# Kernel optimization log

Hardware: AMD Instinct MI355X
Metric: run time of the kernel (lower is better)

Reference implementation:

```python
import jax, jax.numpy as jnp
import numpy as np

N = 50000   # nodes
E = 800000  # edges (before self loops)
NEG_SLOPE = 0.2
EPS_BN = 1e-5
EPS_SM = 1e-16  # PyG softmax denominator epsilon


def gat_conv(x, src, dst, W, att_src, att_dst, bias, heads, ch):
    n = x.shape[0]
    xh = (x @ W).reshape(n, heads, ch)                       # [N,H,C]
    a_src = jnp.sum(xh * att_src, axis=-1)                   # [N,H]
    a_dst = jnp.sum(xh * att_dst, axis=-1)                   # [N,H]
    e = a_src[src] + a_dst[dst]                              # [E,H]
    e = jax.nn.leaky_relu(e, NEG_SLOPE)
    m = jax.ops.segment_max(e, dst, num_segments=n)          # segment softmax
    ex = jnp.exp(e - m[dst])
    denom = jax.ops.segment_sum(ex, dst, num_segments=n)
    alpha = ex / (denom[dst] + EPS_SM)                       # [E,H]
    msg = alpha[:, :, None] * xh[src]                        # [E,H,C]
    out = jax.ops.segment_sum(msg, dst, num_segments=n)      # [N,H,C]
    return out.reshape(n, heads * ch) + bias


def batch_norm(x, gamma, beta):
    mu = jnp.mean(x, axis=0)
    var = jnp.mean((x - mu) ** 2, axis=0)
    return (x - mu) * jax.lax.rsqrt(var + EPS_BN) * gamma + beta


def setup_inputs() -> dict:
    key = jax.random.key(0)
    ks = jax.random.split(key, 16)
    d = {}
    d['x'] = jax.random.normal(ks[0], (N, 128), jnp.float32)
    d['edge_index'] = jax.random.randint(ks[1], (2, E), 0, N, dtype=jnp.int64)
    d['W1'] = jax.random.normal(ks[2], (128, 256), jnp.float32) * 0.1
    d['as1'] = jax.random.normal(ks[3], (2, 128), jnp.float32) * 0.1
    d['ad1'] = jax.random.normal(ks[4], (2, 128), jnp.float32) * 0.1
    d['b1'] = jax.random.normal(ks[5], (256,), jnp.float32) * 0.1
    d['g1'] = jnp.ones((256,), jnp.float32)
    d['be1'] = jnp.zeros((256,), jnp.float32)
    d['W2'] = jax.random.normal(ks[6], (256, 128), jnp.float32) * 0.1
    d['as2'] = jax.random.normal(ks[7], (2, 64), jnp.float32) * 0.1
    d['ad2'] = jax.random.normal(ks[8], (2, 64), jnp.float32) * 0.1
    d['b2'] = jax.random.normal(ks[9], (128,), jnp.float32) * 0.1
    d['g2'] = jnp.ones((128,), jnp.float32)
    d['be2'] = jnp.zeros((128,), jnp.float32)
    d['W3'] = jax.random.normal(ks[10], (128, 128), jnp.float32) * 0.1
    d['as3'] = jax.random.normal(ks[11], (2, 64), jnp.float32) * 0.1
    d['ad3'] = jax.random.normal(ks[12], (2, 64), jnp.float32) * 0.1
    d['b3'] = jax.random.normal(ks[13], (128,), jnp.float32) * 0.1
    d['lw'] = jax.random.normal(ks[14], (128, 64), jnp.float32) * 0.1
    d['lb'] = jnp.zeros((64,), jnp.float32)
    return d


def reference(x, edge_index, W1, as1, ad1, b1, g1, be1,
              W2, as2, ad2, b2, g2, be2,
              W3, as3, ad3, b3, lw, lb):
    # add self loops (PyG GATConv default add_self_loops=True)
    loops = jnp.arange(N, dtype=edge_index.dtype)
    src = jnp.concatenate([edge_index[0], loops])
    dst = jnp.concatenate([edge_index[1], loops])

    h = jax.nn.relu(gat_conv(x, src, dst, W1, as1, ad1, b1, 2, 128))   # [N,256]
    h = batch_norm(h, g1, be1)
    h = jax.nn.relu(gat_conv(h, src, dst, W2, as2, ad2, b2, 2, 64))    # [N,128]
    h = batch_norm(h, g2, be2)
    h = jax.nn.relu(gat_conv(h, src, dst, W3, as3, ad3, b3, 2, 64))    # [N,128]
    return h @ lw + lb                                                 # [N,64]
```

## Files before the change

kernel.cpp:

```cpp
#include <hip/hip_runtime.h>
#include <hip/hip_bf16.h>

#define NEG_SLOPE 0.2f
#define EPS_BN 1e-5f
#define EPS_SM 1e-16f
#define CAP 128

typedef __bf16 bf16x8 __attribute__((ext_vector_type(8)));
typedef __bf16 bf16x4 __attribute__((ext_vector_type(4)));
typedef float floatx4 __attribute__((ext_vector_type(4)));

__device__ __forceinline__ float leaky(float x) { return x > 0.f ? x : NEG_SLOPE * x; }

__global__ void k_init(const int* __restrict__ ei, int* __restrict__ flag,
                       int* __restrict__ zbase, int zwords, int e) {
    if (blockIdx.x == 0) {
        __shared__ int cnt_s[256];
        int i = threadIdx.x;
        int nz = (2 * i + 1 < 2 * e && ei[2 * i + 1] != 0) ? 1 : 0;
        cnt_s[i] = nz;
        __syncthreads();
        for (int off = 128; off > 0; off >>= 1) {
            if (i < off) cnt_s[i] += cnt_s[i + off];
            __syncthreads();
        }
        if (i == 0) *flag = (cnt_s[0] < 128) ? 1 : 0;
        return;
    }
    int g = (blockIdx.x - 1) * 256 + threadIdx.x;
    int stride = (gridDim.x - 1) * 256;
    for (int k = g; k < zwords; k += stride) zbase[k] = 0;
}

__global__ void k_hist_wconv(const int* __restrict__ ei, const int* __restrict__ flag,
                             int* __restrict__ deg, int* __restrict__ col, int e, int ebase,
                             const float* __restrict__ W1, __bf16* __restrict__ Wb1,
                             const float* __restrict__ W2, __bf16* __restrict__ Wb2,
                             const float* __restrict__ W3, __bf16* __restrict__ Wb3) {
    int g = threadIdx.x + blockIdx.x * blockDim.x;
    if (g < e) {
        bool is64 = (*flag) != 0;
        int s = is64 ? ei[2 * g] : ei[g];
        int d = is64 ? ei[2 * (e + g)] : ei[e + g];
        int r = atomicAdd(&deg[d], 1);
        if (r < CAP) col[((size_t)d << 7) + r] = s;
    } else {
        int idx = g - ebase;
        if (idx >= 0 && idx < 32768) {
            int mm = idx >> 7, kk = idx & 127;
            Wb1[idx] = (__bf16)W1[(size_t)kk * 256 + mm];
        } else if (idx < 65536) {
            int i2 = idx - 32768;
            int mm = i2 >> 8, kk = i2 & 255;
            Wb2[i2] = (__bf16)W2[(size_t)kk * 128 + mm];
        } else if (idx < 81920) {
            int i3 = idx - 65536;
            int mm = i3 >> 7, kk = i3 & 127;
            Wb3[i3] = (__bf16)W3[(size_t)kk * 128 + mm];
        }
    }
}

template <int K, int LC, bool BF16IN, int NT>
__global__ __launch_bounds__(256) void k_gemm(const void* __restrict__ Ain,
                                              const __bf16* __restrict__ Bt,
                                              __bf16* __restrict__ Cb, int n, int M,
                                              const float* __restrict__ bnsums,
                                              const float* __restrict__ gam,
                                              const float* __restrict__ bet,
                                              const float* __restrict__ att_s,
                                              const float* __restrict__ att_d,
                                              float* __restrict__ asrc,
                                              float* __restrict__ adst) {
    __shared__ __align__(16) __bf16 As[128][72];
    __shared__ __align__(16) __bf16 Bs[NT * 16][72];
    __shared__ float sc_lds[K], sh_lds[K];
    const int row0 = blockIdx.y * 128, col0 = blockIdx.x * (NT * 16);
    const int lane = threadIdx.x & 63, w = threadIdx.x >> 6;
    const int m = lane & 15, quad = lane >> 4;

    if (bnsums) {
        for (int c = threadIdx.x; c < K; c += 256) {
            float mean = bnsums[c] / n;
            float var = bnsums[256 + c] / n - mean * mean;
            float sc = gam[c] * rsqrtf(var + EPS_BN);
            sc_lds[c] = sc;
            sh_lds[c] = bet[c] - mean * sc;
        }
        __syncthreads();
    }

    floatx4 acc[2][NT];
#pragma unroll
    for (int i = 0; i < 2; ++i)
#pragma unroll
        for (int j = 0; j < NT; ++j) acc[i][j] = (floatx4)0.f;

    const int sr = threadIdx.x >> 1;
    const int sk = (threadIdx.x & 1) * 32;

    for (int kc = 0; kc < K; kc += 64) {
        {
            int grow = row0 + sr;
            if (grow < n) {
                if (BF16IN) {
                    const __bf16* p = (const __bf16*)Ain + (size_t)grow * K + kc + sk;
#pragma unroll
                    for (int q = 0; q < 4; ++q) {
                        bf16x8 vv = *reinterpret_cast<const bf16x8*>(p + q * 8);
                        if (bnsums) {
                            int c = kc + sk + q * 8;
                            bf16x8 r;
#pragma unroll
                            for (int e2 = 0; e2 < 8; ++e2)
                                r[e2] = (__bf16)((float)vv[e2] * sc_lds[c + e2] + sh_lds[c + e2]);
                            vv = r;
                        }
                        *reinterpret_cast<bf16x8*>(&As[sr][sk + q * 8]) = vv;
                    }
                } else {
                    const float* p = (const float*)Ain + (size_t)grow * K + kc + sk;
#pragma unroll
                    for (int q = 0; q < 8; ++q) {
                        float4 v = *reinterpret_cast<const float4*>(p + q * 4);
                        bf16x4 cv = {(__bf16)v.x, (__bf16)v.y, (__bf16)v.z, (__bf16)v.w};
                        *reinterpret_cast<bf16x4*>(&As[sr][sk + q * 4]) = cv;
                    }
                }
            } else {
#pragma unroll
                for (int q = 0; q < 4; ++q)
                    *reinterpret_cast<bf16x8*>(&As[sr][sk + q * 8]) = (bf16x8)(__bf16)0.f;
            }
        }
        if (NT == 8) {
            const __bf16* p = Bt + (size_t)(col0 + sr) * K + kc + sk;
#pragma unroll
            for (int q = 0; q < 4; ++q)
                *reinterpret_cast<bf16x8*>(&Bs[sr][sk + q * 8]) =
                    *reinterpret_cast<const bf16x8*>(p + q * 8);
        } else {
            int sr4 = threadIdx.x >> 2, sk4 = (threadIdx.x & 3) * 16;
            const __bf16* p = Bt + (size_t)(col0 + sr4) * K + kc + sk4;
            *reinterpret_cast<bf16x8*>(&Bs[sr4][sk4]) = *reinterpret_cast<const bf16x8*>(p);
            *reinterpret_cast<bf16x8*>(&Bs[sr4][sk4 + 8]) = *reinterpret_cast<const bf16x8*>(p + 8);
        }
        __syncthreads();
#pragma unroll
        for (int ks = 0; ks < 64; ks += 32) {
            bf16x8 a0 = *reinterpret_cast<const bf16x8*>(&As[w * 32 + m][ks + quad * 8]);
            bf16x8 a1 = *reinterpret_cast<const bf16x8*>(&As[w * 32 + 16 + m][ks + quad * 8]);
#pragma unroll
            for (int nt = 0; nt < NT; ++nt) {
                bf16x8 b = *reinterpret_cast<const bf16x8*>(&Bs[nt * 16 + m][ks + quad * 8]);
                acc[0][nt] = __builtin_amdgcn_mfma_f32_16x16x32_bf16(a0, b, acc[0][nt], 0, 0, 0);
                acc[1][nt] = __builtin_amdgcn_mfma_f32_16x16x32_bf16(a1, b, acc[1][nt], 0, 0, 0);
            }
        }
        __syncthreads();
    }
#pragma unroll
    for (int mt = 0; mt < 2; ++mt)
#pragma unroll
        for (int nt = 0; nt < NT; ++nt)
#pragma unroll
            for (int r = 0; r < 4; ++r) {
                int row = row0 + w * 32 + mt * 16 + quad * 4 + r;
                if (row < n) Cb[(size_t)row * M + col0 + nt * 16 + m] = (__bf16)acc[mt][nt][r];
            }
    {
        float asv[NT], adv[NT];
#pragma unroll
        for (int nt = 0; nt < NT; ++nt) {
            int c = col0 + nt * 16 + m;
            asv[nt] = att_s[c];
            adv[nt] = att_d[c];
        }
        const int h = (col0 >> LC) & 1;
#pragma unroll
        for (int mt = 0; mt < 2; ++mt)
#pragma unroll
            for (int r = 0; r < 4; ++r) {
                int row = row0 + w * 32 + mt * 16 + quad * 4 + r;
                float pa = 0.f, pb = 0.f;
#pragma unroll
                for (int nt = 0; nt < NT; ++nt) {
                    float v = acc[mt][nt][r];
                    pa += v * asv[nt];
                    pb += v * adv[nt];
                }
#pragma unroll
                for (int off = 1; off <= 8; off <<= 1) {
                    pa += __shfl_xor(pa, off);
                    pb += __shfl_xor(pb, off);
                }
                if (m == 0 && row < n) {
                    asrc[2 * row + h] = pa;
                    adst[2 * row + h] = pb;
                }
            }
    }
}

__global__ __launch_bounds__(256) void k_lin(const float* __restrict__ A,
                                             const float* __restrict__ lw,
                                             const float* __restrict__ lb,
                                             float* __restrict__ out, int n) {
    __shared__ __align__(16) __bf16 Ahi[64][136];
    __shared__ __align__(16) __bf16 Alo[64][136];
    __shared__ __align__(16) __bf16 Bhi[64][136];
    const int row0 = blockIdx.x * 64;
    const int lane = threadIdx.x & 63, w = threadIdx.x >> 6;
    const int m = lane & 15, quad = lane >> 4;
    floatx4 acc[4];
#pragma unroll
    for (int i = 0; i < 4; ++i) acc[i] = (floatx4)0.f;
    {
        int sr = threadIdx.x >> 2, sk0 = (threadIdx.x & 3) * 32;
        int grow = row0 + sr;
#pragma unroll
        for (int q = 0; q < 8; ++q) {
            float4 v = make_float4(0.f, 0.f, 0.f, 0.f);
            if (grow < n) v = *reinterpret_cast<const float4*>(A + (size_t)grow * 128 + sk0 + q * 4);
            float vv[4] = {v.x, v.y, v.z, v.w};
#pragma unroll
            for (int i = 0; i < 4; ++i) {
                __bf16 h = (__bf16)vv[i];
                Ahi[sr][sk0 + q * 4 + i] = h;
                Alo[sr][sk0 + q * 4 + i] = (__bf16)(vv[i] - (float)h);
            }
        }
    }
    {
        int k0 = threadIdx.x >> 1, m0 = (threadIdx.x & 1) * 32;
#pragma unroll
        for (int q = 0; q < 8; ++q) {
            float4 v = *reinterpret_cast<const float4*>(lw + (size_t)k0 * 64 + m0 + q * 4);
            float vv[4] = {v.x, v.y, v.z, v.w};
#pragma unroll
            for (int i = 0; i < 4; ++i) Bhi[m0 + q * 4 + i][k0] = (__bf16)vv[i];
        }
    }
    __syncthreads();
#pragma unroll
    for (int ks = 0; ks < 128; ks += 32) {
        bf16x8 ah = *reinterpret_cast<const bf16x8*>(&Ahi[w * 16 + m][ks + quad * 8]);
        bf16x8 al = *reinterpret_cast<const bf16x8*>(&Alo[w * 16 + m][ks + quad * 8]);
#pragma unroll
        for (int nt = 0; nt < 4; ++nt) {
            bf16x8 bh = *reinterpret_cast<const bf16x8*>(&Bhi[nt * 16 + m][ks + quad * 8]);
            acc[nt] = __builtin_amdgcn_mfma_f32_16x16x32_bf16(ah, bh, acc[nt], 0, 0, 0);
            acc[nt] = __builtin_amdgcn_mfma_f32_16x16x32_bf16(al, bh, acc[nt], 0, 0, 0);
        }
    }
#pragma unroll
    for (int nt = 0; nt < 4; ++nt)
#pragma unroll
        for (int r = 0; r < 4; ++r) {
            int row = row0 + w * 16 + quad * 4 + r;
            int c = nt * 16 + m;
            if (row < n) out[(size_t)row * 64 + c] = acc[nt][r] + lb[c];
        }
}

template <int C, bool OUTBF16>
__global__ __launch_bounds__(256) void k_agg(const __bf16* __restrict__ xh,
                                             const float* __restrict__ asrc,
                                             const float* __restrict__ adst,
                                             const int* __restrict__ degv,
                                             const int* __restrict__ col,
                                             const float* __restrict__ bias,
                                             void* __restrict__ outv, int n) {
    constexpr int F = 2 * C;
    constexpr int G = F / 8;
    constexpr int NG = 64 / G;
    constexpr int GSH = (G == 32) ? 5 : 4;
    __shared__ float4 slots[4][64];
    const int widx = threadIdx.x >> 6;
    const int node = blockIdx.x * 4 + widx;
    const int lane = threadIdx.x & 63;
    if (node >= n) return;
    const int t = lane & (G - 1);
    const int g = lane >> GSH;
    const bool h1 = (t * 8) >= C;
    const char* xbt = (const char*)xh + t * 16;
    const int* crow = col + ((size_t)node << 7);
    const int deg = min(degv[node], CAP);
    const float2 adv = *reinterpret_cast<const float2*>(adst + 2 * node);
    const float2 asv = *reinterpret_cast<const float2*>(asrc + 2 * node);
    const float es0 = leaky(asv.x + adv.x), es1 = leaky(asv.y + adv.y);
    bf16x8 vself = *reinterpret_cast<const bf16x8*>(xbt + (size_t)node * (2 * F));
    float acc[8] = {};
    float d0 = 0.f, d1 = 0.f;
    for (int base = 0; base < deg; base += 64) {
        const int cnt = min(64, deg - base);
        float4 sv = make_float4(0.f, 0.f, 0.f, 0.f);
        if (lane < cnt) {
            int s = crow[base + lane];
            float2 av = *reinterpret_cast<const float2*>(asrc + 2 * s);
            float w0 = __expf(leaky(av.x + adv.x));
            float w1 = __expf(leaky(av.y + adv.y));
            d0 += w0; d1 += w1;
            sv = make_float4(__int_as_float(s * (F * 2)), w0, w1, 0.f);
        }
        slots[widx][lane] = sv;
        for (int j = g; j < cnt; j += 8 * NG) {
            unsigned uo[8];
            float wv[8];
#pragma unroll
            for (int i = 0; i < 8; ++i) {
                float4 s = slots[widx][j + i * NG];
                uo[i] = (unsigned)__float_as_int(s.x);
                wv[i] = h1 ? s.z : s.y;
            }
            bf16x8 v[8];
#pragma unroll
            for (int i = 0; i < 8; ++i)
                v[i] = *reinterpret_cast<const bf16x8*>(xbt + uo[i]);
#pragma unroll
            for (int i = 0; i < 8; ++i)
#pragma unroll
                for (int q = 0; q < 8; ++q) acc[q] += wv[i] * (float)v[i][q];
        }
    }
#pragma unroll
    for (int off = 1; off <= 32; off <<= 1) {
        d0 += __shfl_xor(d0, off);
        d1 += __shfl_xor(d1, off);
    }
#pragma unroll
    for (int q = 0; q < 8; ++q) {
#pragma unroll
        for (int off = G; off < 64; off <<= 1) acc[q] += __shfl_xor(acc[q], off);
    }
    float exs0 = __expf(es0), exs1 = __expf(es1);
    d0 += exs0; d1 += exs1;
    {
        float ws = h1 ? exs1 : exs0;
#pragma unroll
        for (int q = 0; q < 8; ++q) acc[q] += ws * (float)vself[q];
    }
    float inv = 1.0f / ((h1 ? d1 : d0) + EPS_SM);
    float o[8];
#pragma unroll
    for (int q = 0; q < 8; ++q) o[q] = fmaxf(acc[q] * inv + bias[t * 8 + q], 0.f);
    if (g == 0) {
        if constexpr (OUTBF16) {
            __bf16* po = (__bf16*)outv + (size_t)node * F + t * 8;
            bf16x8 st;
#pragma unroll
            for (int q = 0; q < 8; ++q) st[q] = (__bf16)o[q];
            *reinterpret_cast<bf16x8*>(po) = st;
        } else {
            float* po = (float*)outv + (size_t)node * F + t * 8;
            *reinterpret_cast<float4*>(po) = make_float4(o[0], o[1], o[2], o[3]);
            *reinterpret_cast<float4*>(po + 4) = make_float4(o[4], o[5], o[6], o[7]);
        }
    }
}

template <typename T>
__global__ void k_bn_stats(const T* __restrict__ x, float* __restrict__ sums,
                           float* __restrict__ sqs, int n, int f) {
    int c = threadIdx.x;
    float s = 0.f, q = 0.f;
    for (int r = blockIdx.x; r < n; r += gridDim.x) {
        float v = (float)x[(size_t)r * f + c];
        s += v; q += v * v;
    }
    atomicAdd(&sums[c], s);
    atomicAdd(&sqs[c], q);
}

extern "C" void kernel_launch(void* const* d_in, const int* in_sizes, int n_in,
                              void* d_out, int out_size, void* d_ws, size_t ws_size,
                              hipStream_t stream) {
    const float* x   = (const float*)d_in[0];
    const int*   ei  = (const int*)d_in[1];
    const float* W1  = (const float*)d_in[2];
    const float* as1 = (const float*)d_in[3];
    const float* ad1 = (const float*)d_in[4];
    const float* b1  = (const float*)d_in[5];
    const float* g1  = (const float*)d_in[6];
    const float* be1 = (const float*)d_in[7];
    const float* W2  = (const float*)d_in[8];
    const float* as2 = (const float*)d_in[9];
    const float* ad2 = (const float*)d_in[10];
    const float* b2  = (const float*)d_in[11];
    const float* g2  = (const float*)d_in[12];
    const float* be2 = (const float*)d_in[13];
    const float* W3  = (const float*)d_in[14];
    const float* as3 = (const float*)d_in[15];
    const float* ad3 = (const float*)d_in[16];
    const float* b3  = (const float*)d_in[17];
    const float* lw  = (const float*)d_in[18];
    const float* lb  = (const float*)d_in[19];
    float* outp = (float*)d_out;

    const int n = in_sizes[0] / 128;
    const int e = in_sizes[1] / 2;

    char* w = (char*)d_ws;
    size_t off = 0;
    auto alloc = [&](size_t bytes) -> void* {
        void* p = w + off;
        off += (bytes + 255) & ~(size_t)255;
        return p;
    };
    __bf16* xhb = (__bf16*)alloc((size_t)n * 256 * 2);
    __bf16* h1b = (__bf16*)alloc((size_t)n * 256 * 2);
    __bf16* h2b = (__bf16*)alloc((size_t)n * 128 * 2);
    float*  h3f = (float*)alloc((size_t)n * 128 * 4);
    int* colb   = (int*)alloc((size_t)n * CAP * 4);
    __bf16* Wb1 = (__bf16*)alloc(256 * 128 * 2);
    __bf16* Wb2 = (__bf16*)alloc(128 * 256 * 2);
    __bf16* Wb3 = (__bf16*)alloc(128 * 128 * 2);
    int* flag   = (int*)alloc(256);
    float* as1p = (float*)alloc((size_t)n * 2 * 4);
    float* ad1p = (float*)alloc((size_t)n * 2 * 4);
    float* as2p = (float*)alloc((size_t)n * 2 * 4);
    float* ad2p = (float*)alloc((size_t)n * 2 * 4);
    float* as3p = (float*)alloc((size_t)n * 2 * 4);
    float* ad3p = (float*)alloc((size_t)n * 2 * 4);
    char* zb_begin = (char*)(w + off);
    int* deg    = (int*)alloc((size_t)n * 4);
    float* bn1  = (float*)alloc(512 * 4);
    float* bn2  = (float*)alloc(512 * 4);
    char* zb_end = (char*)(w + off);
    const int zwords = (int)((zb_end - zb_begin) / 4);

    k_init<<<65, 256, 0, stream>>>(ei, flag, (int*)zb_begin, zwords, e);

    const int ebase = ((e + 255) / 256) * 256;
    const int histblocks = ebase / 256 + 320;
    k_hist_wconv<<<histblocks, 256, 0, stream>>>(ei, flag, deg, colb, e, ebase,
                                                 W1, Wb1, W2, Wb2, W3, Wb3);

    const int nwb = (n + 3) / 4;
    const int nrow = (n + 127) / 128;

    k_gemm<128, 7, false, 8><<<dim3(2, nrow), 256, 0, stream>>>(
        x, Wb1, xhb, n, 256, nullptr, nullptr, nullptr, as1, ad1, as1p, ad1p);
    k_agg<128, true><<<nwb, 256, 0, stream>>>(xhb, as1p, ad1p, deg, colb, b1, h1b, n);
    k_bn_stats<__bf16><<<256, 256, 0, stream>>>(h1b, bn1, bn1 + 256, n, 256);

    k_gemm<256, 6, true, 4><<<dim3(2, nrow), 256, 0, stream>>>(
        h1b, Wb2, xhb, n, 128, bn1, g1, be1, as2, ad2, as2p, ad2p);
    k_agg<64, true><<<nwb, 256, 0, stream>>>(xhb, as2p, ad2p, deg, colb, b2, h2b, n);
    k_bn_stats<__bf16><<<256, 128, 0, stream>>>(h2b, bn2, bn2 + 256, n, 128);

    k_gemm<128, 6, true, 4><<<dim3(2, nrow), 256, 0, stream>>>(
        h2b, Wb3, xhb, n, 128, bn2, g2, be2, as3, ad3, as3p, ad3p);
    k_agg<64, false><<<nwb, 256, 0, stream>>>(xhb, as3p, ad3p, deg, colb, b3, h3f, n);

    k_lin<<<(n + 63) / 64, 256, 0, stream>>>(h3f, lw, lb, outp, n);
}
```

Before: 482.0 us.

## Fuse edge histogram with first GEMM and pad degree counters

Moves the weight bf16 conversion into the init kernel and merges the edge histogram/CSR fill with the first-layer GEMM (including the attention projections) into one launch, so two independent phases share a single grid. Degree counters are padded to one per 64-byte stride to cut atomic contention and false sharing. The aggregation inner loop is rebuilt with split offset and weight LDS arrays and an unroll of 4 instead of 8, with padded slots pointing at the node itself so tail lanes need no branch. The costs are a larger degree array to zero, less memory-level parallelism per iteration in aggregation, and a new hand-written GEMM path for layer 1.

```diff
diff --git a/kernel.cpp b/kernel.cpp
--- a/kernel.cpp
+++ b/kernel.cpp
@@ -5,6 +5,7 @@
 #define EPS_BN 1e-5f
 #define EPS_SM 1e-16f
 #define CAP 128
+#define DEGS 16
 
 typedef __bf16 bf16x8 __attribute__((ext_vector_type(8)));
 typedef __bf16 bf16x4 __attribute__((ext_vector_type(4)));
@@ -13,7 +14,10 @@
 __device__ __forceinline__ float leaky(float x) { return x > 0.f ? x : NEG_SLOPE * x; }
 
 __global__ void k_init(const int* __restrict__ ei, int* __restrict__ flag,
-                       int* __restrict__ zbase, int zwords, int e) {
+                       int* __restrict__ zbase, int zwords, int e,
+                       const float* __restrict__ W1, __bf16* __restrict__ Wb1,
+                       const float* __restrict__ W2, __bf16* __restrict__ Wb2,
+                       const float* __restrict__ W3, __bf16* __restrict__ Wb3) {
     if (blockIdx.x == 0) {
         __shared__ int cnt_s[256];
         int i = threadIdx.x;
@@ -27,26 +31,9 @@
         if (i == 0) *flag = (cnt_s[0] < 128) ? 1 : 0;
         return;
     }
-    int g = (blockIdx.x - 1) * 256 + threadIdx.x;
-    int stride = (gridDim.x - 1) * 256;
-    for (int k = g; k < zwords; k += stride) zbase[k] = 0;
-}
-
-__global__ void k_hist_wconv(const int* __restrict__ ei, const int* __restrict__ flag,
-                             int* __restrict__ deg, int* __restrict__ col, int e, int ebase,
-                             const float* __restrict__ W1, __bf16* __restrict__ Wb1,
-                             const float* __restrict__ W2, __bf16* __restrict__ Wb2,
-                             const float* __restrict__ W3, __bf16* __restrict__ Wb3) {
-    int g = threadIdx.x + blockIdx.x * blockDim.x;
-    if (g < e) {
-        bool is64 = (*flag) != 0;
-        int s = is64 ? ei[2 * g] : ei[g];
-        int d = is64 ? ei[2 * (e + g)] : ei[e + g];
-        int r = atomicAdd(&deg[d], 1);
-        if (r < CAP) col[((size_t)d << 7) + r] = s;
-    } else {
-        int idx = g - ebase;
-        if (idx >= 0 && idx < 32768) {
+    if (blockIdx.x >= 129) {
+        int idx = (blockIdx.x - 129) * 256 + threadIdx.x;
+        if (idx < 32768) {
             int mm = idx >> 7, kk = idx & 127;
             Wb1[idx] = (__bf16)W1[(size_t)kk * 256 + mm];
         } else if (idx < 65536) {
@@ -58,6 +45,121 @@
             int mm = i3 >> 7, kk = i3 & 127;
             Wb3[i3] = (__bf16)W3[(size_t)kk * 128 + mm];
         }
+        return;
+    }
+    int g = (blockIdx.x - 1) * 256 + threadIdx.x;
+    const int stride = 128 * 256;
+    for (int k = g; k < zwords; k += stride) zbase[k] = 0;
+}
+
+__global__ __launch_bounds__(256) void k_hist_gemm1(
+        const int* __restrict__ ei, const int* __restrict__ flag,
+        int* __restrict__ deg, int* __restrict__ col, int e, int ng1,
+        const float* __restrict__ x, const __bf16* __restrict__ Bt,
+        __bf16* __restrict__ xhb, int n,
+        const float* __restrict__ att_s, const float* __restrict__ att_d,
+        float* __restrict__ asrc, float* __restrict__ adst) {
+    __shared__ __align__(16) __bf16 As[128][72];
+    __shared__ __align__(16) __bf16 Bs[128][72];
+    if ((int)blockIdx.x >= ng1) {
+        int g = (blockIdx.x - ng1) * 256 + threadIdx.x;
+        if (g < e) {
+            bool is64 = (*flag) != 0;
+            int s = is64 ? ei[2 * g] : ei[g];
+            int d = is64 ? ei[2 * (e + g)] : ei[e + g];
+            int r = atomicAdd(&deg[(size_t)d * DEGS], 1);
+            if (r < CAP) col[((size_t)d << 7) + r] = s;
+        }
+        return;
+    }
+    const int row0 = (blockIdx.x >> 1) * 128, col0 = (blockIdx.x & 1) * 128;
+    const int lane = threadIdx.x & 63, w = threadIdx.x >> 6;
+    const int m = lane & 15, quad = lane >> 4;
+    floatx4 acc[2][8];
+#pragma unroll
+    for (int i = 0; i < 2; ++i)
+#pragma unroll
+        for (int j = 0; j < 8; ++j) acc[i][j] = (floatx4)0.f;
+    const int sr = threadIdx.x >> 1;
+    const int sk = (threadIdx.x & 1) * 32;
+    for (int kc = 0; kc < 128; kc += 64) {
+        {
+            int grow = row0 + sr;
+            if (grow < n) {
+                const float* p = x + (size_t)grow * 128 + kc + sk;
+#pragma unroll
+                for (int q = 0; q < 8; ++q) {
+                    float4 v = *reinterpret_cast<const float4*>(p + q * 4);
+                    bf16x4 cv = {(__bf16)v.x, (__bf16)v.y, (__bf16)v.z, (__bf16)v.w};
+                    *reinterpret_cast<bf16x4*>(&As[sr][sk + q * 4]) = cv;
+                }
+            } else {
+#pragma unroll
+                for (int q = 0; q < 4; ++q)
+                    *reinterpret_cast<bf16x8*>(&As[sr][sk + q * 8]) = (bf16x8)(__bf16)0.f;
+            }
+        }
+        {
+            const __bf16* p = Bt + (size_t)(col0 + sr) * 128 + kc + sk;
+#pragma unroll
+            for (int q = 0; q < 4; ++q)
+                *reinterpret_cast<bf16x8*>(&Bs[sr][sk + q * 8]) =
+                    *reinterpret_cast<const bf16x8*>(p + q * 8);
+        }
+        __syncthreads();
+#pragma unroll
+        for (int ks = 0; ks < 64; ks += 32) {
+            bf16x8 a0 = *reinterpret_cast<const bf16x8*>(&As[w * 32 + m][ks + quad * 8]);
+            bf16x8 a1 = *reinterpret_cast<const bf16x8*>(&As[w * 32 + 16 + m][ks + quad * 8]);
+#pragma unroll
+            for (int nt = 0; nt < 8; ++nt) {
+                bf16x8 b = *reinterpret_cast<const bf16x8*>(&Bs[nt * 16 + m][ks + quad * 8]);
+                acc[0][nt] = __builtin_amdgcn_mfma_f32_16x16x32_bf16(a0, b, acc[0][nt], 0, 0, 0);
+                acc[1][nt] = __builtin_amdgcn_mfma_f32_16x16x32_bf16(a1, b, acc[1][nt], 0, 0, 0);
+            }
+        }
+        __syncthreads();
+    }
+#pragma unroll
+    for (int mt = 0; mt < 2; ++mt)
+#pragma unroll
+        for (int nt = 0; nt < 8; ++nt)
+#pragma unroll
+            for (int r = 0; r < 4; ++r) {
+                int row = row0 + w * 32 + mt * 16 + quad * 4 + r;
+                if (row < n) xhb[(size_t)row * 256 + col0 + nt * 16 + m] = (__bf16)acc[mt][nt][r];
+            }
+    {
+        float asv[8], adv[8];
+#pragma unroll
+        for (int nt = 0; nt < 8; ++nt) {
+            int c = col0 + nt * 16 + m;
+            asv[nt] = att_s[c];
+            adv[nt] = att_d[c];
+        }
+        const int h = (col0 >> 7) & 1;
+#pragma unroll
+        for (int mt = 0; mt < 2; ++mt)
+#pragma unroll
+            for (int r = 0; r < 4; ++r) {
+                int row = row0 + w * 32 + mt * 16 + quad * 4 + r;
+                float pa = 0.f, pb = 0.f;
+#pragma unroll
+                for (int nt = 0; nt < 8; ++nt) {
+                    float v = acc[mt][nt][r];
+                    pa += v * asv[nt];
+                    pb += v * adv[nt];
+                }
+#pragma unroll
+                for (int off = 1; off <= 8; off <<= 1) {
+                    pa += __shfl_xor(pa, off);
+                    pb += __shfl_xor(pb, off);
+                }
+                if (m == 0 && row < n) {
+                    asrc[2 * row + h] = pa;
+                    adst[2 * row + h] = pb;
+                }
+            }
     }
 }
 
@@ -275,7 +377,8 @@
     constexpr int G = F / 8;
     constexpr int NG = 64 / G;
     constexpr int GSH = (G == 32) ? 5 : 4;
-    __shared__ float4 slots[4][64];
+    __shared__ int sA[4][80];
+    __shared__ float2 sW[4][80];
     const int widx = threadIdx.x >> 6;
     const int node = blockIdx.x * 4 + widx;
     const int lane = threadIdx.x & 63;
@@ -283,44 +386,44 @@
     const int t = lane & (G - 1);
     const int g = lane >> GSH;
     const bool h1 = (t * 8) >= C;
+    const int selfoff = node * (F * 2);
+    if (lane >= 48) { sA[widx][lane + 16] = selfoff; sW[widx][lane + 16] = make_float2(0.f, 0.f); }
     const char* xbt = (const char*)xh + t * 16;
     const int* crow = col + ((size_t)node << 7);
-    const int deg = min(degv[node], CAP);
+    const int deg = min(degv[(size_t)node * DEGS], CAP);
     const float2 adv = *reinterpret_cast<const float2*>(adst + 2 * node);
     const float2 asv = *reinterpret_cast<const float2*>(asrc + 2 * node);
     const float es0 = leaky(asv.x + adv.x), es1 = leaky(asv.y + adv.y);
-    bf16x8 vself = *reinterpret_cast<const bf16x8*>(xbt + (size_t)node * (2 * F));
+    bf16x8 vself = *reinterpret_cast<const bf16x8*>(xbt + selfoff);
     float acc[8] = {};
     float d0 = 0.f, d1 = 0.f;
     for (int base = 0; base < deg; base += 64) {
         const int cnt = min(64, deg - base);
-        float4 sv = make_float4(0.f, 0.f, 0.f, 0.f);
+        int s = (lane < cnt) ? crow[base + lane] : node;
+        sA[widx][lane] = s * (F * 2);
+        float2 av = *reinterpret_cast<const float2*>(asrc + 2 * s);
+        float w0 = 0.f, w1 = 0.f;
         if (lane < cnt) {
-            int s = crow[base + lane];
-            float2 av = *reinterpret_cast<const float2*>(asrc + 2 * s);
-            float w0 = __expf(leaky(av.x + adv.x));
-            float w1 = __expf(leaky(av.y + adv.y));
+            w0 = __expf(leaky(av.x + adv.x));
+            w1 = __expf(leaky(av.y + adv.y));
             d0 += w0; d1 += w1;
-            sv = make_float4(__int_as_float(s * (F * 2)), w0, w1, 0.f);
-        }
-        slots[widx][lane] = sv;
-        for (int j = g; j < cnt; j += 8 * NG) {
-            unsigned uo[8];
-            float wv[8];
-#pragma unroll
-            for (int i = 0; i < 8; ++i) {
-                float4 s = slots[widx][j + i * NG];
-                uo[i] = (unsigned)__float_as_int(s.x);
-                wv[i] = h1 ? s.z : s.y;
-            }
-            bf16x8 v[8];
-#pragma unroll
-            for (int i = 0; i < 8; ++i)
-                v[i] = *reinterpret_cast<const bf16x8*>(xbt + uo[i]);
-#pragma unroll
-            for (int i = 0; i < 8; ++i)
-#pragma unroll
-                for (int q = 0; q < 8; ++q) acc[q] += wv[i] * (float)v[i][q];
+        }
+        sW[widx][lane] = make_float2(w0, w1);
+        for (int j = g; j < cnt; j += 4 * NG) {
+            int o0 = sA[widx][j], o1 = sA[widx][j + NG], o2 = sA[widx][j + 2 * NG], o3 = sA[widx][j + 3 * NG];
+            bf16x8 v0 = *reinterpret_cast<const bf16x8*>(xbt + o0);
+            bf16x8 v1 = *reinterpret_cast<const bf16x8*>(xbt + o1);
+            bf16x8 v2 = *reinterpret_cast<const bf16x8*>(xbt + o2);
+            bf16x8 v3 = *reinterpret_cast<const bf16x8*>(xbt + o3);
+            float2 x0 = sW[widx][j], x1 = sW[widx][j + NG], x2 = sW[widx][j + 2 * NG], x3 = sW[widx][j + 3 * NG];
+            float w0 = h1 ? x0.y : x0.x;
+            float w1 = h1 ? x1.y : x1.x;
+            float w2 = h1 ? x2.y : x2.x;
+            float w3 = h1 ? x3.y : x3.x;
+#pragma unroll
+            for (int q = 0; q < 8; ++q)
+                acc[q] += w0 * (float)v0[q] + w1 * (float)v1[q] +
+                          w2 * (float)v2[q] + w3 * (float)v3[q];
         }
     }
 #pragma unroll
@@ -423,24 +526,23 @@
     float* as3p = (float*)alloc((size_t)n * 2 * 4);
     float* ad3p = (float*)alloc((size_t)n * 2 * 4);
     char* zb_begin = (char*)(w + off);
-    int* deg    = (int*)alloc((size_t)n * 4);
+    int* deg    = (int*)alloc((size_t)n * DEGS * 4);
     float* bn1  = (float*)alloc(512 * 4);
     float* bn2  = (float*)alloc(512 * 4);
     char* zb_end = (char*)(w + off);
     const int zwords = (int)((zb_end - zb_begin) / 4);
 
-    k_init<<<65, 256, 0, stream>>>(ei, flag, (int*)zb_begin, zwords, e);
-
-    const int ebase = ((e + 255) / 256) * 256;
-    const int histblocks = ebase / 256 + 320;
-    k_hist_wconv<<<histblocks, 256, 0, stream>>>(ei, flag, deg, colb, e, ebase,
-                                                 W1, Wb1, W2, Wb2, W3, Wb3);
+    k_init<<<449, 256, 0, stream>>>(ei, flag, (int*)zb_begin, zwords, e,
+                                    W1, Wb1, W2, Wb2, W3, Wb3);
+
+    const int nrow = (n + 127) / 128;
+    const int ng1 = 2 * nrow;
+    const int eb = ((e + 255) / 256);
+    k_hist_gemm1<<<ng1 + eb, 256, 0, stream>>>(ei, flag, deg, colb, e, ng1,
+                                               x, Wb1, xhb, n, as1, ad1, as1p, ad1p);
 
     const int nwb = (n + 3) / 4;
-    const int nrow = (n + 127) / 128;
-
-    k_gemm<128, 7, false, 8><<<dim3(2, nrow), 256, 0, stream>>>(
-        x, Wb1, xhb, n, 256, nullptr, nullptr, nullptr, as1, ad1, as1p, ad1p);
+
     k_agg<128, true><<<nwb, 256, 0, stream>>>(xhb, as1p, ad1p, deg, colb, b1, h1b, n);
     k_bn_stats<__bf16><<<256, 256, 0, stream>>>(h1b, bn1, bn1 + 256, n, 256);
 
```

Result: faster. 464.3 us (-3.7%).
